# Performance work log

Measured on AMD Instinct MI355X. Metric: run time of the kernel, lower is better.

## Reference

```python
import jax, jax.numpy as jnp
import numpy as np

N = 768
SINGLE_DIM = 384
PAIR_DIM = 128
D = 16      # proj_dim per head
H = 12      # n_heads
P = 4       # n_query_points
PV = 8      # n_point_values


def _random_rotations(key, n):
    a = jax.random.normal(key, (n, 3, 3), dtype=jnp.float32)
    q, r = jnp.linalg.qr(a)
    d = jnp.sign(jnp.diagonal(r, axis1=-2, axis2=-1))
    q = q * d[:, None, :]
    det = jnp.linalg.det(q)
    return q * jnp.where(det < 0, -1.0, 1.0)[:, None, None]


def setup_inputs() -> dict:
    key = jax.random.key(0)
    ks = jax.random.split(key, 12)
    s = 0.02
    return {
        "single_rep": jax.random.normal(ks[0], (N, SINGLE_DIM), dtype=jnp.float32),
        "pair_rep": jax.random.normal(ks[1], (N, N, PAIR_DIM), dtype=jnp.float32),
        "rotations": _random_rotations(ks[2], N),
        "translations": jax.random.normal(ks[3], (N, 3), dtype=jnp.float32),
        "Wqkv": s * jax.random.normal(ks[4], (SINGLE_DIM, 3 * H * D), dtype=jnp.float32),
        "Wb": s * jax.random.normal(ks[5], (PAIR_DIM, H), dtype=jnp.float32),
        "Wqk_pts": s * jax.random.normal(ks[6], (SINGLE_DIM, 2 * H * P * 3), dtype=jnp.float32),
        "Wv_pts": s * jax.random.normal(ks[7], (SINGLE_DIM, H * PV * 3), dtype=jnp.float32),
        "gamma": 0.1 * jax.random.normal(ks[8], (H,), dtype=jnp.float32),
        "Wout": s * jax.random.normal(ks[9], (H * (PAIR_DIM + D + PV * 3 + PV), SINGLE_DIM), dtype=jnp.float32),
        "bout": jnp.zeros((SINGLE_DIM,), dtype=jnp.float32),
    }


def _apply_frames(rot, trans, pts):
    # pts: [N, P, H, 3] -> R @ pt + t per residue (dim 0)
    return jnp.einsum('nba,npha->nphb', rot, pts) + trans[:, None, None, :]


def _apply_frames_inv(rot, trans, pts):
    # R^T (pt - t)
    return jnp.einsum('nab,npha->nphb', rot, pts - trans[:, None, None, :])


def reference(single_rep, pair_rep, rotations, translations,
              Wqkv, Wb, Wqk_pts, Wv_pts, gamma, Wout, bout):
    n = single_rep.shape[0]
    sqrt_inv_dim = 1.0 / np.sqrt(D).astype(np.float32)
    w_C = np.sqrt(2.0 / (9.0 * P)).astype(np.float32)
    w_L = np.sqrt(1.0 / 3.0).astype(np.float32)

    qkv = single_rep @ Wqkv                       # [N, 3*H*D]
    q, k, v = jnp.split(qkv, 3, axis=-1)
    q = q.reshape(n, D, H)
    k = k.reshape(n, D, H)
    v = v.reshape(n, D, H)

    b = pair_rep @ Wb                             # [N, N, H]

    qk_pts = single_rep @ Wqk_pts
    q_pts, k_pts = jnp.split(qk_pts, 2, axis=-1)
    q_pts = jnp.moveaxis(q_pts.reshape(n, P, 3, H), -1, -2)   # [N, P, H, 3]
    k_pts = jnp.moveaxis(k_pts.reshape(n, P, 3, H), -1, -2)
    v_pts = jnp.moveaxis((single_rep @ Wv_pts).reshape(n, PV, 3, H), -1, -2)  # [N, PV, H, 3]

    qg = _apply_frames(rotations, translations, q_pts)  # [N, P, H, 3]
    kg = _apply_frames(rotations, translations, k_pts)

    # sum_{p,t} ||qg_i - kg_j||^2 via expansion (avoids [N,N,P,H,3])
    q_sq = jnp.sum(qg * qg, axis=(1, 3))                # [N, H]
    k_sq = jnp.sum(kg * kg, axis=(1, 3))                # [N, H]
    cross = jnp.einsum('ipht,jpht->ijh', qg, kg)        # [N, N, H]
    dist_logits = q_sq[:, None, :] + k_sq[None, :, :] - 2.0 * cross

    dp_logits = sqrt_inv_dim * jnp.einsum('idh,jdh->ijh', q, k) + b
    scale = gamma * (w_C / 2.0)                          # [H]
    a = jax.nn.softmax(w_L * (dp_logits - scale * dist_logits), axis=1)  # [N, N, H]

    out_pair = jnp.einsum('ijh,ijz->izh', a, pair_rep)   # [N, pair_dim, H]
    out_value = jnp.einsum('ijh,jdh->idh', a, v)          # [N, D, H]

    vg = _apply_frames(rotations, translations, v_pts)    # [N, PV, H, 3]
    op = jnp.einsum('ijh,jpht->ipht', a, vg)              # [N, PV, H, 3]
    out_points = _apply_frames_inv(rotations, translations, op)
    out_points_norm = jnp.linalg.norm(out_points, axis=-1)  # [N, PV, H]

    out = jnp.concatenate([
        out_pair.reshape(n, -1),
        out_value.reshape(n, -1),
        out_points.reshape(n, -1),
        out_points_norm.reshape(n, -1),
    ], axis=1)
    return out @ Wout + bout
```

## Files before the change

### kernel.cpp

```cpp
#include <hip/hip_runtime.h>
#include <math.h>

#define NN 768
#define SD 384
#define HH 12

#define W_L 0.57735026918962576f
#define W_C 0.23570226039551584f

typedef __attribute__((ext_vector_type(8))) short short8;
typedef __attribute__((ext_vector_type(4))) float floatx4;
typedef unsigned short ushort_t;
typedef unsigned int uint_t;

static __device__ __forceinline__ ushort_t f2bf(float f) {
  union { float f; uint_t u; } v; v.f = f;
  uint_t r = (v.u + 0x7FFFu + ((v.u >> 16) & 1u)) >> 16;
  return (ushort_t)r;
}

__global__ __launch_bounds__(256) void k1a_gemm(
    const float* __restrict__ single, const float* __restrict__ Wqkv,
    const float* __restrict__ Wqk, const float* __restrict__ Wvp,
    float* __restrict__ raw)
{
  __shared__ float Al[64][17];
  __shared__ float Bl[16][68];
  const int tid = threadIdx.x;
  const int bm = blockIdx.x / 18, bn = blockIdx.x % 18;
  const int tr = tid >> 4, tc = tid & 15;

  const int bcol = bn*64 + (tid & 15)*4;
  const float* Wsrc; int wstride;
  if (bcol < 576)      { Wsrc = Wqkv + bcol;        wstride = 576; }
  else if (bcol < 864) { Wsrc = Wqk  + (bcol-576);  wstride = 288; }
  else                 { Wsrc = Wvp  + (bcol-864);  wstride = 288; }
  const int brow = tid >> 4;
  const int ar = tid >> 2, ac = (tid & 3)*4;

  float4 acc0 = {0,0,0,0}, acc1 = {0,0,0,0}, acc2 = {0,0,0,0}, acc3 = {0,0,0,0};

  for (int kc = 0; kc < 24; ++kc) {
    __syncthreads();
    *(float4*)&Al[ar][ac] = *(const float4*)(single + (size_t)(bm*64+ar)*SD + kc*16 + ac);
    *(float4*)&Bl[brow][(tid&15)*4] = *(const float4*)(Wsrc + (size_t)(kc*16+brow)*wstride);
    __syncthreads();
    #pragma unroll
    for (int kk = 0; kk < 16; ++kk) {
      float a0 = Al[tr*4+0][kk], a1 = Al[tr*4+1][kk], a2 = Al[tr*4+2][kk], a3 = Al[tr*4+3][kk];
      float4 bv = *(float4*)&Bl[kk][tc*4];
      acc0.x += a0*bv.x; acc0.y += a0*bv.y; acc0.z += a0*bv.z; acc0.w += a0*bv.w;
      acc1.x += a1*bv.x; acc1.y += a1*bv.y; acc1.z += a1*bv.z; acc1.w += a1*bv.w;
      acc2.x += a2*bv.x; acc2.y += a2*bv.y; acc2.z += a2*bv.z; acc2.w += a2*bv.w;
      acc3.x += a3*bv.x; acc3.y += a3*bv.y; acc3.z += a3*bv.z; acc3.w += a3*bv.w;
    }
  }
  float* o = raw + (size_t)(bm*64 + tr*4)*1152 + bn*64 + tc*4;
  *(float4*)(o)            = acc0;
  *(float4*)(o + 1152)     = acc1;
  *(float4*)(o + 2*1152)   = acc2;
  *(float4*)(o + 3*1152)   = acc3;
}

__global__ __launch_bounds__(256) void k1b_pack(
    const float* __restrict__ raw_g, const float* __restrict__ rot,
    const float* __restrict__ trans, const float* __restrict__ gamma,
    float* __restrict__ Qt, ushort_t* __restrict__ Ktb, float* __restrict__ vv)
{
  __shared__ float raw[4][1152];
  __shared__ float gbuf[4][16][HH][3];
  const int tid = threadIdx.x;
  const int i0 = blockIdx.x * 4;

  for (int s = tid; s < 4*288; s += 256) {
    int r = s / 288, q = s % 288;
    *(float4*)(&raw[r][q*4]) = *(const float4*)(raw_g + (size_t)(i0+r)*1152 + q*4);
  }
  __syncthreads();

  for (int s = tid; s < 4*576; s += 256) {
    int r = s / 576, cc = s % 576;
    int d = (cc % 192) / HH, h = cc % HH;
    int i = i0 + r;
    float val = raw[r][cc];
    if (cc < 192)       Qt[(size_t)i*384 + h*32 + d] = 0.25f*W_L*val;
    else if (cc < 384)  Ktb[(size_t)i*384 + h*32 + d] = f2bf(val);
    else                vv[(size_t)i*480 + h*40 + d] = val;
  }
  for (int s = tid; s < 768; s += 256) {
    int r = s / 192, rem = s % 192;
    int slot = rem / HH, h = rem % HH;
    int i = i0 + r;
    int base;
    if (slot < 4) base = 576 + slot*36;
    else if (slot < 8) base = 720 + (slot-4)*36;
    else base = 864 + (slot-8)*36;
    float x0 = raw[r][base + 0*12 + h];
    float x1 = raw[r][base + 1*12 + h];
    float x2 = raw[r][base + 2*12 + h];
    const float* R = rot + (size_t)i*9;
    const float* T = trans + (size_t)i*3;
    float g0 = R[0]*x0 + R[1]*x1 + R[2]*x2 + T[0];
    float g1 = R[3]*x0 + R[4]*x1 + R[5]*x2 + T[1];
    float g2 = R[6]*x0 + R[7]*x1 + R[8]*x2 + T[2];
    gbuf[r][slot][h][0]=g0; gbuf[r][slot][h][1]=g1; gbuf[r][slot][h][2]=g2;
    if (slot < 4) {
      float sc2 = 2.0f*W_L*(gamma[h]*W_C*0.5f);
      float* q = Qt + (size_t)i*384 + h*32 + 16 + slot*3;
      q[0]=sc2*g0; q[1]=sc2*g1; q[2]=sc2*g2;
    } else if (slot < 8) {
      ushort_t* k = Ktb + (size_t)i*384 + h*32 + 16 + (slot-4)*3;
      k[0]=f2bf(g0); k[1]=f2bf(g1); k[2]=f2bf(g2);
    } else {
      float* vp = vv + (size_t)i*480 + h*40 + 16 + (slot-8)*3;
      vp[0]=g0; vp[1]=g1; vp[2]=g2;
    }
  }
  __syncthreads();
  for (int s = tid; s < 96; s += 256) {
    int r = s / 24, rem = s % 24;
    int h = rem / 2, qk = rem % 2;
    int i = i0 + r;
    float sum = 0;
    int b0 = qk ? 4 : 0;
    for (int p = 0; p < 4; ++p)
      for (int t = 0; t < 3; ++t) { float g = gbuf[r][b0+p][h][t]; sum += g*g; }
    float sc = gamma[h]*W_C*0.5f;
    if (qk == 0) {
      float* q = Qt + (size_t)i*384 + h*32;
      q[28] = -W_L*sc; q[29] = -W_L*sc*sum; q[30] = 0.f; q[31] = 0.f;
    } else {
      ushort_t* k = Ktb + (size_t)i*384 + h*32;
      k[28] = f2bf(sum); k[29] = f2bf(1.f); k[30] = 0; k[31] = 0;
    }
  }
}

__global__ __launch_bounds__(256) void k2m(
    const float* __restrict__ pair, const float* __restrict__ Wb,
    const float* __restrict__ Qt, const ushort_t* __restrict__ Ktb,
    const float* __restrict__ vv, const float* __restrict__ rot,
    const float* __restrict__ trans, float* __restrict__ C2)
{
  __shared__ ushort_t Tjz[2][32*136];
  __shared__ ushort_t Tzj[2][128*40];
  __shared__ ushort_t WbT[16*136];
  __shared__ ushort_t PT[16*40];
  __shared__ float pl[12*33];
  __shared__ float lL[32*17];
  __shared__ float Qrow[384];
  __shared__ float smm[16], sms[16], scl[16];
  __shared__ float oacc[480];

  const int tid = threadIdx.x;
  const int i = blockIdx.x;
  const int lane = tid & 63;
  const int wv = tid >> 6;
  const int sj = tid & 31, szq = tid >> 5;
  const int co = lane & 15, gg = lane >> 4;

  for (int s = tid; s < 1536; s += 256) {
    int z = s / 12, h = s % 12;
    WbT[h*136 + z] = f2bf(W_L * Wb[s]);
  }
  for (int s = tid; s < 4*136; s += 256) WbT[(12 + s/136)*136 + (s%136)] = 0;
  for (int s = tid; s < 16*40; s += 256) PT[s] = 0;
  for (int s = tid; s < 384; s += 256) Qrow[s] = Qt[(size_t)i*384 + s];
  if (tid < 16) { smm[tid] = -1e30f; sms[tid] = 0.f; scl[tid] = 0.f; }
  __syncthreads();

  short8 myQ; short8 z8;
  #pragma unroll
  for (int s = 0; s < 8; ++s) z8[s] = 0;
  #pragma unroll
  for (int s = 0; s < 8; ++s)
    myQ[s] = (co < 12) ? (short)f2bf(Qrow[co*32 + gg*8 + s]) : (short)0;

  const float* psrc = pair + (size_t)i*NN*128;

  float4 cur[4], nxt[4];
  {
    const float* s0 = psrc + (size_t)sj*128 + szq*16;
    cur[0] = *(const float4*)(s0);     cur[1] = *(const float4*)(s0+4);
    cur[2] = *(const float4*)(s0+8);   cur[3] = *(const float4*)(s0+12);
  }

  floatx4 accP[8];
  #pragma unroll
  for (int n = 0; n < 8; ++n) { accP[n][0]=0.f; accP[n][1]=0.f; accP[n][2]=0.f; accP[n][3]=0.f; }
  float accB[4] = {0,0,0,0};
  const int tid2 = tid - 128;
  const int c0 = (tid2 >= 0 && tid2 < 120) ? tid2*4 : 0;
  const int hB = c0 / 40;

  for (int t = 0; t <= 24; ++t) {
    const int buf = t & 1;
    if (t < 24) {
      if (t < 23) {
        const float* sn = psrc + (size_t)(t+1)*32*128 + (size_t)sj*128 + szq*16;
        nxt[0] = *(const float4*)(sn);     nxt[1] = *(const float4*)(sn+4);
        nxt[2] = *(const float4*)(sn+8);   nxt[3] = *(const float4*)(sn+12);
      }
      const float* cf = (const float*)cur;
      ushort_t bb[16];
      #pragma unroll
      for (int e = 0; e < 16; ++e) bb[e] = f2bf(cf[e]);
      short8 w0, w1;
      #pragma unroll
      for (int e = 0; e < 8; ++e) { w0[e] = (short)bb[e]; w1[e] = (short)bb[8+e]; }
      *(short8*)&Tjz[buf][sj*136 + szq*16]     = w0;
      *(short8*)&Tjz[buf][sj*136 + szq*16 + 8] = w1;
      #pragma unroll
      for (int e = 0; e < 16; ++e) Tzj[buf][(szq*16 + e)*40 + sj] = bb[e];
    }
    __syncthreads();

    if (t < 24 && wv == 1) {
      #pragma unroll
      for (int Mt = 0; Mt < 2; ++Mt) {
        floatx4 D; D[0]=0.f; D[1]=0.f; D[2]=0.f; D[3]=0.f;
        const int jr = Mt*16 + co;
        #pragma unroll
        for (int kt = 0; kt < 4; ++kt) {
          short8 a = *(const short8*)&Tjz[buf][jr*136 + kt*32 + gg*8];
          short8 b = *(const short8*)&WbT[co*136 + kt*32 + gg*8];
          D = __builtin_amdgcn_mfma_f32_16x16x32_bf16(a, b, D, 0, 0, 0);
        }
        const ushort_t* kr = Ktb + (size_t)(t*32 + jr)*384;
        #pragma unroll
        for (int kt = 0; kt < 12; ++kt) {
          short8 a = *(const short8*)(kr + kt*32 + gg*8);
          short8 b = (co == kt) ? myQ : z8;
          D = __builtin_amdgcn_mfma_f32_16x16x32_bf16(a, b, D, 0, 0, 0);
        }
        #pragma unroll
        for (int r = 0; r < 4; ++r) lL[(Mt*16 + gg*4 + r)*17 + co] = D[r];
      }
    }
    if (t > 0) {
      const int pbuf = (t-1) & 1;
      if (wv == 0) {
        float s4[4];
        #pragma unroll
        for (int r = 0; r < 4; ++r) s4[r] = scl[gg*4 + r];
        short8 aP = *(const short8*)&PT[co*40 + gg*8];
        #pragma unroll
        for (int Nt = 0; Nt < 8; ++Nt) {
          floatx4 aa = accP[Nt];
          aa[0]*=s4[0]; aa[1]*=s4[1]; aa[2]*=s4[2]; aa[3]*=s4[3];
          short8 bT = *(const short8*)&Tzj[pbuf][(Nt*16 + co)*40 + gg*8];
          accP[Nt] = __builtin_amdgcn_mfma_f32_16x16x32_bf16(aP, bT, aa, 0, 0, 0);
        }
      } else if (wv >= 2 && tid2 < 120) {
        float sc = scl[hB];
        accB[0]*=sc; accB[1]*=sc; accB[2]*=sc; accB[3]*=sc;
        const int j0 = (t-1)*32;
        const float* vp = vv + (size_t)j0*480 + c0;
        #pragma unroll 4
        for (int jj = 0; jj < 32; ++jj) {
          float p = pl[hB*33 + jj];
          float4 v = *(const float4*)(vp + (size_t)jj*480);
          accB[0] += p*v.x; accB[1] += p*v.y; accB[2] += p*v.z; accB[3] += p*v.w;
        }
      }
    }
    __syncthreads();

    if (t < 24 && wv == 0 && lane < 48) {
      const int h = lane >> 2, q = lane & 3;
      float v[8];
      #pragma unroll
      for (int e = 0; e < 8; ++e) v[e] = lL[(q*8 + e)*17 + h];
      float mt = fmaxf(fmaxf(fmaxf(v[0],v[1]),fmaxf(v[2],v[3])),
                       fmaxf(fmaxf(v[4],v[5]),fmaxf(v[6],v[7])));
      mt = fmaxf(mt, __shfl_xor(mt, 1));
      mt = fmaxf(mt, __shfl_xor(mt, 2));
      float mo = smm[h];
      float mn = fmaxf(mo, mt);
      float sc = __expf(mo - mn);
      float ps = 0.f;
      #pragma unroll
      for (int e = 0; e < 8; ++e) {
        float p = __expf(v[e] - mn);
        pl[h*33 + q*8 + e] = p;
        PT[h*40 + q*8 + e] = f2bf(p);
        ps += p;
      }
      ps += __shfl_xor(ps, 1);
      ps += __shfl_xor(ps, 2);
      if (q == 0) { sms[h] = sms[h]*sc + ps; smm[h] = mn; scl[h] = sc; }
    }
    __syncthreads();

    if (t < 23) { cur[0]=nxt[0]; cur[1]=nxt[1]; cur[2]=nxt[2]; cur[3]=nxt[3]; }
  }

  if (wv == 0) {
    float* o = C2 + (size_t)i*2112;
    #pragma unroll
    for (int Nt = 0; Nt < 8; ++Nt) {
      #pragma unroll
      for (int r = 0; r < 4; ++r) {
        int h = gg*4 + r;
        if (h < 12) o[(Nt*16 + co)*12 + h] = accP[Nt][r] / sms[h];
      }
    }
  } else if (wv >= 2 && tid2 < 120) {
    float inv = 1.0f / sms[hB];
    #pragma unroll
    for (int e = 0; e < 4; ++e) oacc[c0 + e] = accB[e]*inv;
  }
  __syncthreads();

  if (tid < 96) {
    const int pp = tid / 12, h = tid % 12;
    const float* R = rot + (size_t)i*9;
    const float* T = trans + (size_t)i*3;
    float x0 = oacc[h*40+16+pp*3+0] - T[0];
    float x1 = oacc[h*40+16+pp*3+1] - T[1];
    float x2 = oacc[h*40+16+pp*3+2] - T[2];
    float y0 = R[0]*x0 + R[3]*x1 + R[6]*x2;
    float y1 = R[1]*x0 + R[4]*x1 + R[7]*x2;
    float y2 = R[2]*x0 + R[5]*x1 + R[8]*x2;
    float* o = C2 + (size_t)i*2112;
    o[1728 + pp*36 + h*3 + 0] = y0;
    o[1728 + pp*36 + h*3 + 1] = y1;
    o[1728 + pp*36 + h*3 + 2] = y2;
    o[2016 + pp*12 + h] = sqrtf(y0*y0 + y1*y1 + y2*y2);
  } else if (tid < 192) {
    const int c = tid - 96;
    float* o = C2 + (size_t)i*2112 + 1536;
    o[c]      = oacc[(c%12)*40 + (c/12)];
    o[c+96]   = oacc[((c+96)%12)*40 + ((c+96)/12)];
  }
}

__global__ __launch_bounds__(256) void k5_out(
    const float* __restrict__ C2, const float* __restrict__ Wout,
    const float* __restrict__ bout, float* __restrict__ out)
{
  __shared__ float Al[32*68];
  __shared__ float Bl[64*36];
  const int tid = threadIdx.x;
  const int bm = blockIdx.x / 12, bn = blockIdx.x % 12;
  const int tr = tid / 16, tc = tid % 16;
  float acc00=0, acc01=0, acc10=0, acc11=0;
  for (int kc = 0; kc < 33; ++kc) {
    __syncthreads();
    for (int s = tid; s < 512; s += 256) {
      int row = s / 16, kq = s % 16;
      *(float4*)(&Al[row*68 + kq*4]) =
        *(const float4*)(C2 + (size_t)(bm*32+row)*2112 + kc*64 + kq*4);
    }
    for (int s = tid; s < 512; s += 256) {
      int kk = s / 8, cq = s % 8;
      *(float4*)(&Bl[kk*36 + cq*4]) =
        *(const float4*)(Wout + (size_t)(kc*64+kk)*384 + bn*32 + cq*4);
    }
    __syncthreads();
    for (int kk = 0; kk < 64; ++kk) {
      float a0 = Al[(tr*2)*68 + kk], a1 = Al[(tr*2+1)*68 + kk];
      float b0 = Bl[kk*36 + tc*2], b1 = Bl[kk*36 + tc*2 + 1];
      acc00 += a0*b0; acc01 += a0*b1;
      acc10 += a1*b0; acc11 += a1*b1;
    }
  }
  int r0 = bm*32 + tr*2, c0 = bn*32 + tc*2;
  out[(size_t)r0*384 + c0]       = acc00 + bout[c0];
  out[(size_t)r0*384 + c0+1]     = acc01 + bout[c0+1];
  out[(size_t)(r0+1)*384 + c0]   = acc10 + bout[c0];
  out[(size_t)(r0+1)*384 + c0+1] = acc11 + bout[c0+1];
}

extern "C" void kernel_launch(void* const* d_in, const int* in_sizes, int n_in,
                              void* d_out, int out_size, void* d_ws, size_t ws_size,
                              hipStream_t stream)
{
  const float* single = (const float*)d_in[0];
  const float* pair   = (const float*)d_in[1];
  const float* rot    = (const float*)d_in[2];
  const float* trans  = (const float*)d_in[3];
  const float* Wqkv   = (const float*)d_in[4];
  const float* Wb     = (const float*)d_in[5];
  const float* Wqk    = (const float*)d_in[6];
  const float* Wvp    = (const float*)d_in[7];
  const float* gamma  = (const float*)d_in[8];
  const float* Wout   = (const float*)d_in[9];
  const float* bout   = (const float*)d_in[10];

  float* ws   = (float*)d_ws;
  float* raw  = ws;
  float* Qt   = raw + (size_t)768*1152;
  float* vvp  = Qt + (size_t)768*384;
  float* C2   = vvp + (size_t)768*480;
  ushort_t* Ktb = (ushort_t*)(C2 + (size_t)768*2112);
  float* out  = (float*)d_out;

  k1a_gemm<<<dim3(216), dim3(256), 0, stream>>>(single, Wqkv, Wqk, Wvp, raw);
  k1b_pack<<<dim3(192), dim3(256), 0, stream>>>(raw, rot, trans, gamma, Qt, Ktb, vvp);
  k2m<<<dim3(768), dim3(256), 0, stream>>>(pair, Wb, Qt, Ktb, vvp, rot, trans, C2);
  k5_out<<<dim3(288), dim3(256), 0, stream>>>(C2, Wout, bout, out);
}
```

Baseline: 352.5 us.

## Split fused attention kernel into logits, softmax-pairout, and value-point kernels

Replaces the single online-softmax kernel with three passes. The first computes all logits into a global buffer across many small blocks. The second does a full row softmax, stores bf16 probabilities in place, then streams pair_rep again for the pair output. The third computes value and point outputs from the stored probabilities, with the value and point tensors now held in bf16. This removes the serial per-tile softmax dependency and the wave imbalance of the fused loop, at the cost of reading pair_rep twice from HBM and adding extra launches and logit traffic.

```diff
diff --git a/kernel.cpp b/kernel.cpp
--- a/kernel.cpp
+++ b/kernel.cpp
@@ -13,10 +13,16 @@
 typedef unsigned short ushort_t;
 typedef unsigned int uint_t;
 
+__device__ __forceinline__ float wave_max(float v){ for(int o=32;o;o>>=1) v=fmaxf(v,__shfl_xor(v,o)); return v; }
+__device__ __forceinline__ float wave_sum(float v){ for(int o=32;o;o>>=1) v+=__shfl_xor(v,o); return v; }
+
 static __device__ __forceinline__ ushort_t f2bf(float f) {
   union { float f; uint_t u; } v; v.f = f;
   uint_t r = (v.u + 0x7FFFu + ((v.u >> 16) & 1u)) >> 16;
   return (ushort_t)r;
+}
+static __device__ __forceinline__ float bf2f(ushort_t u) {
+  union { uint_t u; float f; } v; v.u = ((uint_t)u) << 16; return v.f;
 }
 
 __global__ __launch_bounds__(256) void k1a_gemm(
@@ -65,7 +71,7 @@
 __global__ __launch_bounds__(256) void k1b_pack(
     const float* __restrict__ raw_g, const float* __restrict__ rot,
     const float* __restrict__ trans, const float* __restrict__ gamma,
-    float* __restrict__ Qt, ushort_t* __restrict__ Ktb, float* __restrict__ vv)
+    float* __restrict__ Qt, ushort_t* __restrict__ Ktb, ushort_t* __restrict__ vvb)
 {
   __shared__ float raw[4][1152];
   __shared__ float gbuf[4][16][HH][3];
@@ -85,7 +91,7 @@
     float val = raw[r][cc];
     if (cc < 192)       Qt[(size_t)i*384 + h*32 + d] = 0.25f*W_L*val;
     else if (cc < 384)  Ktb[(size_t)i*384 + h*32 + d] = f2bf(val);
-    else                vv[(size_t)i*480 + h*40 + d] = val;
+    else                vvb[(size_t)i*480 + h*40 + d] = f2bf(val);
   }
   for (int s = tid; s < 768; s += 256) {
     int r = s / 192, rem = s % 192;
@@ -112,8 +118,8 @@
       ushort_t* k = Ktb + (size_t)i*384 + h*32 + 16 + (slot-4)*3;
       k[0]=f2bf(g0); k[1]=f2bf(g1); k[2]=f2bf(g2);
     } else {
-      float* vp = vv + (size_t)i*480 + h*40 + 16 + (slot-8)*3;
-      vp[0]=g0; vp[1]=g1; vp[2]=g2;
+      ushort_t* vp = vvb + (size_t)i*480 + h*40 + 16 + (slot-8)*3;
+      vp[0]=f2bf(g0); vp[1]=f2bf(g1); vp[2]=f2bf(g2);
     }
   }
   __syncthreads();
@@ -136,202 +142,247 @@
   }
 }
 
-__global__ __launch_bounds__(256) void k2m(
+__global__ __launch_bounds__(256) void k2a_logits(
     const float* __restrict__ pair, const float* __restrict__ Wb,
     const float* __restrict__ Qt, const ushort_t* __restrict__ Ktb,
-    const float* __restrict__ vv, const float* __restrict__ rot,
-    const float* __restrict__ trans, float* __restrict__ C2)
-{
-  __shared__ ushort_t Tjz[2][32*136];
-  __shared__ ushort_t Tzj[2][128*40];
+    float* __restrict__ L)
+{
+  __shared__ ushort_t Tj[64*136];
   __shared__ ushort_t WbT[16*136];
-  __shared__ ushort_t PT[16*40];
-  __shared__ float pl[12*33];
-  __shared__ float lL[32*17];
   __shared__ float Qrow[384];
-  __shared__ float smm[16], sms[16], scl[16];
-  __shared__ float oacc[480];
-
-  const int tid = threadIdx.x;
-  const int i = blockIdx.x;
+  const int tid = threadIdx.x;
+  const int i = blockIdx.x / 12;
+  const int j0 = (blockIdx.x % 12) * 64;
   const int lane = tid & 63;
-  const int wv = tid >> 6;
-  const int sj = tid & 31, szq = tid >> 5;
+  const int w = tid >> 6;
   const int co = lane & 15, gg = lane >> 4;
 
   for (int s = tid; s < 1536; s += 256) {
     int z = s / 12, h = s % 12;
     WbT[h*136 + z] = f2bf(W_L * Wb[s]);
   }
-  for (int s = tid; s < 4*136; s += 256) WbT[(12 + s/136)*136 + (s%136)] = 0;
-  for (int s = tid; s < 16*40; s += 256) PT[s] = 0;
+  for (int s = tid; s < 544; s += 256) WbT[1632 + s] = 0;
   for (int s = tid; s < 384; s += 256) Qrow[s] = Qt[(size_t)i*384 + s];
-  if (tid < 16) { smm[tid] = -1e30f; sms[tid] = 0.f; scl[tid] = 0.f; }
-  __syncthreads();
-
-  short8 myQ; short8 z8;
+
+  const float* src = pair + ((size_t)i*NN + j0)*128;
+  #pragma unroll
+  for (int k = 0; k < 8; ++k) {
+    int f = tid + k*256;
+    int row = f >> 5, zq = f & 31;
+    float4 v = *(const float4*)(src + (size_t)row*128 + zq*4);
+    uint_t u0 = ((uint_t)f2bf(v.y) << 16) | f2bf(v.x);
+    uint_t u1 = ((uint_t)f2bf(v.w) << 16) | f2bf(v.z);
+    uint_t* d = (uint_t*)&Tj[row*136 + zq*4];
+    d[0] = u0; d[1] = u1;
+  }
+  __syncthreads();
+
+  short8 z8, myQ, wb[4];
   #pragma unroll
   for (int s = 0; s < 8; ++s) z8[s] = 0;
   #pragma unroll
   for (int s = 0; s < 8; ++s)
     myQ[s] = (co < 12) ? (short)f2bf(Qrow[co*32 + gg*8 + s]) : (short)0;
-
+  #pragma unroll
+  for (int kt = 0; kt < 4; ++kt)
+    wb[kt] = *(const short8*)&WbT[co*136 + kt*32 + gg*8];
+
+  const int jb = w*16;
+  floatx4 D; D[0]=0.f; D[1]=0.f; D[2]=0.f; D[3]=0.f;
+  #pragma unroll
+  for (int kt = 0; kt < 4; ++kt) {
+    short8 a = *(const short8*)&Tj[(jb+co)*136 + kt*32 + gg*8];
+    D = __builtin_amdgcn_mfma_f32_16x16x32_bf16(a, wb[kt], D, 0, 0, 0);
+  }
+  const ushort_t* kr = Ktb + (size_t)(j0 + jb + co)*384;
+  #pragma unroll
+  for (int kt = 0; kt < 12; ++kt) {
+    short8 a = *(const short8*)(kr + kt*32 + gg*8);
+    short8 b = (co == kt) ? myQ : z8;
+    D = __builtin_amdgcn_mfma_f32_16x16x32_bf16(a, b, D, 0, 0, 0);
+  }
+  if (co < 12) {
+    float4 st = {D[0], D[1], D[2], D[3]};
+    *(float4*)(L + ((size_t)i*12 + co)*768 + j0 + jb + gg*4) = st;
+  }
+}
+
+__global__ __launch_bounds__(256) void k2b_pairout(
+    const float* __restrict__ pair, float* __restrict__ L,
+    float* __restrict__ C2)
+{
+  __shared__ ushort_t PTb[24*16*32];
+  __shared__ ushort_t Tz[32*134];
+  const int tid = threadIdx.x;
+  const int i = (NN - 1) - blockIdx.x;
+  const int lane = tid & 63;
+  const int w = tid >> 6;
+  const int co = lane & 15, gg = lane >> 4;
+
+  float* Lr = L + (size_t)i*12*768;
+  ushort_t* abr = (ushort_t*)Lr;
+  const int ln = lane;
+  {
+    const int wv = w;
+    #pragma unroll 1
+    for (int m = 0; m < 3; ++m) {
+      int h = wv + 4*m;
+      const float* row = Lr + (size_t)h*768;
+      float mx = -1e30f;
+      for (int jj = ln; jj < 768; jj += 64) mx = fmaxf(mx, row[jj]);
+      mx = wave_max(mx);
+      float sm = 0.f;
+      float ev[12];
+      #pragma unroll
+      for (int k = 0; k < 12; ++k) {
+        float e = __expf(row[ln + 64*k] - mx);
+        ev[k] = e; sm += e;
+      }
+      sm = wave_sum(sm);
+      float inv = 1.0f / sm;
+      #pragma unroll
+      for (int k = 0; k < 12; ++k) {
+        int jj = ln + 64*k;
+        ushort_t a = f2bf(ev[k]*inv);
+        PTb[(jj >> 5)*512 + h*32 + (jj & 31)] = a;
+      }
+      #pragma unroll
+      for (int k = 0; k < 12; ++k) {
+        int jj = ln + 64*k;
+        abr[h*768 + jj] = f2bf(ev[k]*inv);
+      }
+    }
+  }
+  __syncthreads();
+
+  floatx4 accZ[2];
+  #pragma unroll
+  for (int u = 0; u < 2; ++u) { accZ[u][0]=0.f; accZ[u][1]=0.f; accZ[u][2]=0.f; accZ[u][3]=0.f; }
+
+  const int srow = tid >> 5, szq = tid & 31;
   const float* psrc = pair + (size_t)i*NN*128;
 
-  float4 cur[4], nxt[4];
-  {
-    const float* s0 = psrc + (size_t)sj*128 + szq*16;
-    cur[0] = *(const float4*)(s0);     cur[1] = *(const float4*)(s0+4);
-    cur[2] = *(const float4*)(s0+8);   cur[3] = *(const float4*)(s0+12);
-  }
-
-  floatx4 accP[8];
-  #pragma unroll
-  for (int n = 0; n < 8; ++n) { accP[n][0]=0.f; accP[n][1]=0.f; accP[n][2]=0.f; accP[n][3]=0.f; }
-  float accB[4] = {0,0,0,0};
-  const int tid2 = tid - 128;
-  const int c0 = (tid2 >= 0 && tid2 < 120) ? tid2*4 : 0;
-  const int hB = c0 / 40;
-
-  for (int t = 0; t <= 24; ++t) {
-    const int buf = t & 1;
-    if (t < 24) {
-      if (t < 23) {
-        const float* sn = psrc + (size_t)(t+1)*32*128 + (size_t)sj*128 + szq*16;
-        nxt[0] = *(const float4*)(sn);     nxt[1] = *(const float4*)(sn+4);
-        nxt[2] = *(const float4*)(sn+8);   nxt[3] = *(const float4*)(sn+12);
+  float4 pr[4];
+  #pragma unroll
+  for (int k = 0; k < 4; ++k) {
+    int f = tid + k*256;
+    int row = f >> 5, zq = f & 31;
+    pr[k] = *(const float4*)(psrc + (size_t)row*128 + zq*4);
+  }
+
+  #pragma unroll 1
+  for (int t = 0; t < 24; ++t) {
+    #pragma unroll
+    for (int k = 0; k < 4; ++k) {
+      int f = tid + k*256;
+      int row = f >> 5, zq = f & 31;
+      uint_t u0 = ((uint_t)f2bf(pr[k].y) << 16) | f2bf(pr[k].x);
+      uint_t u1 = ((uint_t)f2bf(pr[k].w) << 16) | f2bf(pr[k].z);
+      uint_t* d = (uint_t*)Tz;
+      d[row*67 + zq*2]     = u0;
+      d[row*67 + zq*2 + 1] = u1;
+    }
+    __syncthreads();
+    if (t < 23) {
+      const float* sn = psrc + (size_t)(t+1)*32*128;
+      #pragma unroll
+      for (int k = 0; k < 4; ++k) {
+        int f = tid + k*256;
+        int row = f >> 5, zq = f & 31;
+        pr[k] = *(const float4*)(sn + (size_t)row*128 + zq*4);
       }
-      const float* cf = (const float*)cur;
-      ushort_t bb[16];
+    }
+    short8 aP = *(const short8*)&PTb[t*512 + co*32 + gg*8];
+    #pragma unroll
+    for (int u = 0; u < 2; ++u) {
+      const int n = w*2 + u;
+      short8 bT;
       #pragma unroll
-      for (int e = 0; e < 16; ++e) bb[e] = f2bf(cf[e]);
-      short8 w0, w1;
-      #pragma unroll
-      for (int e = 0; e < 8; ++e) { w0[e] = (short)bb[e]; w1[e] = (short)bb[8+e]; }
-      *(short8*)&Tjz[buf][sj*136 + szq*16]     = w0;
-      *(short8*)&Tjz[buf][sj*136 + szq*16 + 8] = w1;
-      #pragma unroll
-      for (int e = 0; e < 16; ++e) Tzj[buf][(szq*16 + e)*40 + sj] = bb[e];
-    }
-    __syncthreads();
-
-    if (t < 24 && wv == 1) {
-      #pragma unroll
-      for (int Mt = 0; Mt < 2; ++Mt) {
-        floatx4 D; D[0]=0.f; D[1]=0.f; D[2]=0.f; D[3]=0.f;
-        const int jr = Mt*16 + co;
-        #pragma unroll
-        for (int kt = 0; kt < 4; ++kt) {
-          short8 a = *(const short8*)&Tjz[buf][jr*136 + kt*32 + gg*8];
-          short8 b = *(const short8*)&WbT[co*136 + kt*32 + gg*8];
-          D = __builtin_amdgcn_mfma_f32_16x16x32_bf16(a, b, D, 0, 0, 0);
-        }
-        const ushort_t* kr = Ktb + (size_t)(t*32 + jr)*384;
-        #pragma unroll
-        for (int kt = 0; kt < 12; ++kt) {
-          short8 a = *(const short8*)(kr + kt*32 + gg*8);
-          short8 b = (co == kt) ? myQ : z8;
-          D = __builtin_amdgcn_mfma_f32_16x16x32_bf16(a, b, D, 0, 0, 0);
-        }
-        #pragma unroll
-        for (int r = 0; r < 4; ++r) lL[(Mt*16 + gg*4 + r)*17 + co] = D[r];
+      for (int e = 0; e < 8; ++e)
+        bT[e] = (short)Tz[(gg*8 + e)*134 + n*16 + co];
+      accZ[u] = __builtin_amdgcn_mfma_f32_16x16x32_bf16(aP, bT, accZ[u], 0, 0, 0);
+    }
+    __syncthreads();
+  }
+
+  float* o = C2 + (size_t)i*2112;
+  #pragma unroll
+  for (int u = 0; u < 2; ++u) {
+    const int n = w*2 + u;
+    #pragma unroll
+    for (int r = 0; r < 4; ++r) {
+      int h = gg*4 + r;
+      if (h < 12) o[(n*16 + co)*12 + h] = accZ[u][r];
+    }
+  }
+}
+
+__global__ __launch_bounds__(256) void k4_value_points(
+    const float* __restrict__ L, const ushort_t* __restrict__ vvb,
+    const float* __restrict__ rot, const float* __restrict__ trans,
+    float* __restrict__ C2)
+{
+  __shared__ ushort_t abl[12*768];
+  __shared__ ushort_t vt[32*488];
+  __shared__ float oacc[480];
+  const int tid = threadIdx.x;
+  const int i = blockIdx.x;
+  const ushort_t* abr = (const ushort_t*)(L + (size_t)i*12*768);
+
+  for (int s = tid; s < 4608; s += 256)
+    ((uint_t*)abl)[s] = ((const uint_t*)abr)[s];
+
+  const int h = tid / 20, c2 = tid % 20;
+  float acc0 = 0.f, acc1 = 0.f;
+
+  #pragma unroll 1
+  for (int t = 0; t < 24; ++t) {
+    __syncthreads();
+    const ushort_t* src = vvb + (size_t)t*32*480;
+    for (int s = tid; s < 1920; s += 256) {
+      int row = s / 60, cq = s % 60;
+      *(float4*)&vt[row*488 + cq*8] = *(const float4*)(src + (size_t)row*480 + cq*8);
+    }
+    __syncthreads();
+    if (tid < 240) {
+      const int j0 = t*32;
+      #pragma unroll 4
+      for (int jj = 0; jj < 32; ++jj) {
+        float a = bf2f(abl[h*768 + j0 + jj]);
+        uint_t pv = *(const uint_t*)&vt[jj*488 + h*40 + c2*2];
+        acc0 += a * bf2f((ushort_t)(pv & 0xffffu));
+        acc1 += a * bf2f((ushort_t)(pv >> 16));
       }
     }
-    if (t > 0) {
-      const int pbuf = (t-1) & 1;
-      if (wv == 0) {
-        float s4[4];
-        #pragma unroll
-        for (int r = 0; r < 4; ++r) s4[r] = scl[gg*4 + r];
-        short8 aP = *(const short8*)&PT[co*40 + gg*8];
-        #pragma unroll
-        for (int Nt = 0; Nt < 8; ++Nt) {
-          floatx4 aa = accP[Nt];
-          aa[0]*=s4[0]; aa[1]*=s4[1]; aa[2]*=s4[2]; aa[3]*=s4[3];
-          short8 bT = *(const short8*)&Tzj[pbuf][(Nt*16 + co)*40 + gg*8];
-          accP[Nt] = __builtin_amdgcn_mfma_f32_16x16x32_bf16(aP, bT, aa, 0, 0, 0);
-        }
-      } else if (wv >= 2 && tid2 < 120) {
-        float sc = scl[hB];
-        accB[0]*=sc; accB[1]*=sc; accB[2]*=sc; accB[3]*=sc;
-        const int j0 = (t-1)*32;
-        const float* vp = vv + (size_t)j0*480 + c0;
-        #pragma unroll 4
-        for (int jj = 0; jj < 32; ++jj) {
-          float p = pl[hB*33 + jj];
-          float4 v = *(const float4*)(vp + (size_t)jj*480);
-          accB[0] += p*v.x; accB[1] += p*v.y; accB[2] += p*v.z; accB[3] += p*v.w;
-        }
-      }
-    }
-    __syncthreads();
-
-    if (t < 24 && wv == 0 && lane < 48) {
-      const int h = lane >> 2, q = lane & 3;
-      float v[8];
-      #pragma unroll
-      for (int e = 0; e < 8; ++e) v[e] = lL[(q*8 + e)*17 + h];
-      float mt = fmaxf(fmaxf(fmaxf(v[0],v[1]),fmaxf(v[2],v[3])),
-                       fmaxf(fmaxf(v[4],v[5]),fmaxf(v[6],v[7])));
-      mt = fmaxf(mt, __shfl_xor(mt, 1));
-      mt = fmaxf(mt, __shfl_xor(mt, 2));
-      float mo = smm[h];
-      float mn = fmaxf(mo, mt);
-      float sc = __expf(mo - mn);
-      float ps = 0.f;
-      #pragma unroll
-      for (int e = 0; e < 8; ++e) {
-        float p = __expf(v[e] - mn);
-        pl[h*33 + q*8 + e] = p;
-        PT[h*40 + q*8 + e] = f2bf(p);
-        ps += p;
-      }
-      ps += __shfl_xor(ps, 1);
-      ps += __shfl_xor(ps, 2);
-      if (q == 0) { sms[h] = sms[h]*sc + ps; smm[h] = mn; scl[h] = sc; }
-    }
-    __syncthreads();
-
-    if (t < 23) { cur[0]=nxt[0]; cur[1]=nxt[1]; cur[2]=nxt[2]; cur[3]=nxt[3]; }
-  }
-
-  if (wv == 0) {
-    float* o = C2 + (size_t)i*2112;
-    #pragma unroll
-    for (int Nt = 0; Nt < 8; ++Nt) {
-      #pragma unroll
-      for (int r = 0; r < 4; ++r) {
-        int h = gg*4 + r;
-        if (h < 12) o[(Nt*16 + co)*12 + h] = accP[Nt][r] / sms[h];
-      }
-    }
-  } else if (wv >= 2 && tid2 < 120) {
-    float inv = 1.0f / sms[hB];
-    #pragma unroll
-    for (int e = 0; e < 4; ++e) oacc[c0 + e] = accB[e]*inv;
+  }
+  __syncthreads();
+  if (tid < 240) {
+    oacc[h*40 + c2*2]     = acc0;
+    oacc[h*40 + c2*2 + 1] = acc1;
   }
   __syncthreads();
 
   if (tid < 96) {
-    const int pp = tid / 12, h = tid % 12;
+    const int pp = tid / 12, hh = tid % 12;
     const float* R = rot + (size_t)i*9;
     const float* T = trans + (size_t)i*3;
-    float x0 = oacc[h*40+16+pp*3+0] - T[0];
-    float x1 = oacc[h*40+16+pp*3+1] - T[1];
-    float x2 = oacc[h*40+16+pp*3+2] - T[2];
+    float x0 = oacc[hh*40+16+pp*3+0] - T[0];
+    float x1 = oacc[hh*40+16+pp*3+1] - T[1];
+    float x2 = oacc[hh*40+16+pp*3+2] - T[2];
     float y0 = R[0]*x0 + R[3]*x1 + R[6]*x2;
     float y1 = R[1]*x0 + R[4]*x1 + R[7]*x2;
     float y2 = R[2]*x0 + R[5]*x1 + R[8]*x2;
     float* o = C2 + (size_t)i*2112;
-    o[1728 + pp*36 + h*3 + 0] = y0;
-    o[1728 + pp*36 + h*3 + 1] = y1;
-    o[1728 + pp*36 + h*3 + 2] = y2;
-    o[2016 + pp*12 + h] = sqrtf(y0*y0 + y1*y1 + y2*y2);
-  } else if (tid < 192) {
+    o[1728 + pp*36 + hh*3 + 0] = y0;
+    o[1728 + pp*36 + hh*3 + 1] = y1;
+    o[1728 + pp*36 + hh*3 + 2] = y2;
+    o[2016 + pp*12 + hh] = sqrtf(y0*y0 + y1*y1 + y2*y2);
+  } else if (tid >= 96 && tid < 288) {
     const int c = tid - 96;
-    float* o = C2 + (size_t)i*2112 + 1536;
-    o[c]      = oacc[(c%12)*40 + (c/12)];
-    o[c+96]   = oacc[((c+96)%12)*40 + ((c+96)/12)];
+    if (c < 192) {
+      int d = c / 12, hh = c % 12;
+      C2[(size_t)i*2112 + 1536 + d*12 + hh] = oacc[hh*40 + d];
+    }
   }
 }
 
@@ -391,13 +442,16 @@
   float* ws   = (float*)d_ws;
   float* raw  = ws;
   float* Qt   = raw + (size_t)768*1152;
-  float* vvp  = Qt + (size_t)768*384;
-  float* C2   = vvp + (size_t)768*480;
-  ushort_t* Ktb = (ushort_t*)(C2 + (size_t)768*2112);
+  float* C2   = Qt  + (size_t)768*384;
+  float* L    = C2  + (size_t)768*2112;
+  ushort_t* Ktb = (ushort_t*)(L + (size_t)768*12*768);
+  ushort_t* vvb = Ktb + (size_t)768*384;
   float* out  = (float*)d_out;
 
   k1a_gemm<<<dim3(216), dim3(256), 0, stream>>>(single, Wqkv, Wqk, Wvp, raw);
-  k1b_pack<<<dim3(192), dim3(256), 0, stream>>>(raw, rot, trans, gamma, Qt, Ktb, vvp);
-  k2m<<<dim3(768), dim3(256), 0, stream>>>(pair, Wb, Qt, Ktb, vvp, rot, trans, C2);
+  k1b_pack<<<dim3(192), dim3(256), 0, stream>>>(raw, rot, trans, gamma, Qt, Ktb, vvb);
+  k2a_logits<<<dim3(9216), dim3(256), 0, stream>>>(pair, Wb, Qt, Ktb, L);
+  k2b_pairout<<<dim3(768), dim3(256), 0, stream>>>(pair, L, C2);
+  k4_value_points<<<dim3(768), dim3(256), 0, stream>>>(L, vvb, rot, trans, C2);
   k5_out<<<dim3(288), dim3(256), 0, stream>>>(C2, Wout, bout, out);
 }
```

Measured after the change: 390.3 us. 1.11x slower.
